# Optimization experiments

Measured on AMD Instinct MI355X. Metric: run time of the kernel, lower is better.

## Reference

```python
import jax, jax.numpy as jnp
import numpy as np

D_MODEL = 1024
NHEAD = 16
HEAD_DIM = D_MODEL // NHEAD
LN_EPS = 1e-5
ROPE_BASE = 10000.0


def _rope_cos_sin(n, head_dim):
    inv_freq = 1.0 / (ROPE_BASE ** (jnp.arange(0, head_dim, 2, dtype=jnp.float32) / head_dim))
    t = jnp.arange(n, dtype=jnp.float32)
    freqs = jnp.outer(t, inv_freq)  # (N, head_dim//2)
    return jnp.cos(freqs), jnp.sin(freqs)


def _apply_rope(x, cos, sin):
    # x: (B, H, N, hd); cos/sin: (N, hd//2)
    B, H, N, hd = x.shape
    xr = x.reshape(B, H, N, hd // 2, 2)
    x0, x1 = xr[..., 0], xr[..., 1]
    c = cos[None, None]
    s = sin[None, None]
    rot = jnp.stack([x0 * c - x1 * s, x0 * s + x1 * c], axis=-1)
    return rot.reshape(B, H, N, hd)


def setup_inputs() -> dict:
    key = jax.random.key(0)
    ks = jax.random.split(key, 6)
    D = D_MODEL
    scale = 1.0 / np.sqrt(D)
    x = jax.random.normal(ks[0], (2, 2048, D), dtype=jnp.float32)
    Wq = jax.random.normal(ks[1], (D, D), dtype=jnp.float32) * scale
    Wk = jax.random.normal(ks[2], (D, D), dtype=jnp.float32) * scale
    Wv = jax.random.normal(ks[3], (D, D), dtype=jnp.float32) * scale
    Wo = jax.random.normal(ks[4], (D, D), dtype=jnp.float32) * scale
    bq = jnp.zeros((D,), jnp.float32)
    bk = jnp.zeros((D,), jnp.float32)
    bv = jnp.zeros((D,), jnp.float32)
    bo = jnp.zeros((D,), jnp.float32)
    ln_w = jnp.ones((D,), jnp.float32)
    ln_b = jnp.zeros((D,), jnp.float32)
    return {"x": x, "ln_w": ln_w, "ln_b": ln_b, "Wq": Wq, "bq": bq,
            "Wk": Wk, "bk": bk, "Wv": Wv, "bv": bv, "Wo": Wo, "bo": bo}


def reference(x, ln_w, ln_b, Wq, bq, Wk, bk, Wv, bv, Wo, bo):
    B, N, D = x.shape
    H, hd = NHEAD, HEAD_DIM
    # LayerNorm
    mu = jnp.mean(x, axis=-1, keepdims=True)
    var = jnp.mean(jnp.square(x - mu), axis=-1, keepdims=True)
    xn = (x - mu) * jax.lax.rsqrt(var + LN_EPS) * ln_w + ln_b
    # QKV projections -> (B, H, N, hd)
    def proj(W, b):
        return (xn @ W.T + b).reshape(B, N, H, hd).transpose(0, 2, 1, 3)
    q = proj(Wq, bq)
    k = proj(Wk, bk)
    v = proj(Wv, bv)
    cos, sin = _rope_cos_sin(N, hd)
    q = _apply_rope(q, cos, sin)
    k = _apply_rope(k, cos, sin)
    scores = jnp.einsum('bhqd,bhkd->bhqk', q, k) / jnp.sqrt(jnp.float32(hd))
    attn = jax.nn.softmax(scores, axis=-1)
    out = jnp.einsum('bhqk,bhkd->bhqd', attn, v)
    out = out.transpose(0, 2, 1, 3).reshape(B, N, D)
    return x + out @ Wo.T + bo
```

## Files before the change

kernel.cpp:

```cpp
#include <hip/hip_runtime.h>


#define SEQ 2048
#define LN_EPS 1e-5f

using short8 = __attribute__((ext_vector_type(8))) short;
using f32x4  = __attribute__((ext_vector_type(4))) float;
using f32x16 = __attribute__((ext_vector_type(16))) float;

__device__ __forceinline__ unsigned short f2bf(float f) {
  union { float f; unsigned u; } v; v.f = f;
  unsigned r = v.u + 0x7FFFu + ((v.u >> 16) & 1u);
  return (unsigned short)(r >> 16);
}

__device__ __forceinline__ void async16(const void* g, void* l) {
  __builtin_amdgcn_global_load_lds(
      (const __attribute__((address_space(1))) void*)g,
      (__attribute__((address_space(3))) void*)l, 16, 0, 0);
}

__global__ __launch_bounds__(256) void prep_kernel(
    const float* __restrict__ x, const float* __restrict__ lnw, const float* __restrict__ lnb,
    const float* __restrict__ wq, const float* __restrict__ wk,
    const float* __restrict__ wv, const float* __restrict__ wo,
    unsigned short* __restrict__ wqkv, unsigned short* __restrict__ wob,
    unsigned short* __restrict__ xn, float2* __restrict__ tab) {
  const int b = blockIdx.x, t = threadIdx.x;
  if (b < 4096) {
    const int gid = b * 256 + t;
    const int m = gid >> 18, e4 = gid & 262143;
    const float* src = (m == 0) ? wq : (m == 1) ? wk : (m == 2) ? wv : wo;
    const float4 v = ((const float4*)src)[e4];
    ushort4 o; o.x = f2bf(v.x); o.y = f2bf(v.y); o.z = f2bf(v.z); o.w = f2bf(v.w);
    if (m < 3) ((ushort4*)wqkv)[(size_t)m * 262144 + e4] = o;
    else       ((ushort4*)wob)[e4] = o;
  } else if (b < 8192) {
    const int row = b - 4096;
    const float4 v = ((const float4*)(x + (size_t)row * 1024))[t];
    float s  = v.x + v.y + v.z + v.w;
    float s2 = v.x * v.x + v.y * v.y + v.z * v.z + v.w * v.w;
#pragma unroll
    for (int off = 32; off >= 1; off >>= 1) {
      s  += __shfl_xor(s, off);
      s2 += __shfl_xor(s2, off);
    }
    __shared__ float red[8];
    const int lane = t & 63, wave = t >> 6;
    if (lane == 0) { red[wave] = s; red[4 + wave] = s2; }
    __syncthreads();
    s  = red[0] + red[1] + red[2] + red[3];
    s2 = red[4] + red[5] + red[6] + red[7];
    const float mu   = s * (1.0f / 1024.0f);
    const float var  = s2 * (1.0f / 1024.0f) - mu * mu;
    const float rstd = rsqrtf(var + LN_EPS);
    const float4 wv4 = ((const float4*)lnw)[t];
    const float4 bv4 = ((const float4*)lnb)[t];
    ushort4 o;
    o.x = f2bf((v.x - mu) * rstd * wv4.x + bv4.x);
    o.y = f2bf((v.y - mu) * rstd * wv4.y + bv4.y);
    o.z = f2bf((v.z - mu) * rstd * wv4.z + bv4.z);
    o.w = f2bf((v.w - mu) * rstd * wv4.w + bv4.w);
    ((ushort4*)xn)[(size_t)row * 256 + t] = o;
  } else {
    const int gid = (b - 8192) * 256 + t;
    const int pos = gid >> 5, ip = gid & 31;
    const float invf = exp2f((float)ip * -0.4152410118609203f);
    const float fr = (float)pos * invf;
    tab[gid] = make_float2(cosf(fr), sinf(fr));
  }
}

__global__ __launch_bounds__(256, 3) void gemm_qkv_kernel(
    const unsigned short* __restrict__ A,
    const unsigned short* __restrict__ Bw,
    const float* __restrict__ bq, const float* __restrict__ bk, const float* __restrict__ bv,
    const float2* __restrict__ tab,
    unsigned short* __restrict__ qb, unsigned short* __restrict__ kbg,
    unsigned short* __restrict__ vtb) {
  __shared__ unsigned short lA[128 * 64];
  __shared__ unsigned short lB[128 * 64];
  const int tid = threadIdx.x;
  const int lane = tid & 63, wave = tid >> 6;
  const int lr = lane & 15, quad = lane >> 4;
  const int wm = (wave >> 1) * 64, wn = (wave & 1) * 64;
  const int n0 = blockIdx.x * 128, m0 = blockIdx.y * 128;
  const int r7 = lr & 7;
  const int lrow = lane >> 3, lcg = (lane & 7) ^ lrow;
  const int lin = blockIdx.y * gridDim.x + blockIdx.x;
  const int phase = ((lin >> 8) * 5) & 15;

  f32x4 acc[4][4];
#pragma unroll
  for (int i = 0; i < 4; ++i)
#pragma unroll
    for (int j = 0; j < 4; ++j) acc[i][j] = (f32x4){0.f, 0.f, 0.f, 0.f};

  for (int kt = 0; kt < 16; ++kt) {
    const int kofs = ((kt + phase) & 15) * 64;
    __syncthreads();
#pragma unroll
    for (int c = 0; c < 4; ++c) {
      const int chunk = wave * 4 + c;
      const int grow = chunk * 8 + lrow;
      async16(&A[(size_t)(m0 + grow) * 1024 + kofs + lcg * 8], &lA[chunk * 512]);
      async16(&Bw[(size_t)(n0 + grow) * 1024 + kofs + lcg * 8], &lB[chunk * 512]);
    }
    __syncthreads();
#pragma unroll
    for (int kk = 0; kk < 2; ++kk) {
      short8 a[4], b[4];
#pragma unroll
      for (int i = 0; i < 4; ++i)
        a[i] = *(const short8*)&lA[(wm + i * 16 + lr) * 64 + ((kk * 4 + quad) ^ r7) * 8];
#pragma unroll
      for (int j = 0; j < 4; ++j)
        b[j] = *(const short8*)&lB[(wn + j * 16 + lr) * 64 + ((kk * 4 + quad) ^ r7) * 8];
#pragma unroll
      for (int i = 0; i < 4; ++i)
#pragma unroll
        for (int j = 0; j < 4; ++j)
          acc[i][j] = __builtin_amdgcn_mfma_f32_16x16x32_bf16(a[i], b[j], acc[i][j], 0, 0, 0);
    }
  }

  const int which = n0 >> 10;
  const float* bias = (which == 0) ? bq : (which == 1) ? bk : bv;
  const float qs = (which == 0) ? 0.18033688011112042f : 1.0f;
#pragma unroll
  for (int i = 0; i < 4; ++i)
#pragma unroll
    for (int j = 0; j < 4; ++j)
#pragma unroll
      for (int r = 0; r < 4; ++r) {
        const int row = m0 + wm + i * 16 + quad * 4 + r;
        const int col = n0 + wn + j * 16 + lr;
        const int c = col & 1023;
        float val = (acc[i][j][r] + bias[c]) * qs;
        const int head = c >> 6, hd_i = c & 63;
        const int b_ = row >> 11, pos = row & 2047;
        if (which < 2) {
          const float partner = __shfl_xor(val, 1);
          const float2 cs = tab[(pos << 5) + (hd_i >> 1)];
          val = val * cs.x + partner * ((lane & 1) ? cs.y : -cs.y);
        }
        if (which == 2) {
          vtb[((size_t)((b_ * 16 + head) * 64 + hd_i)) * SEQ + pos] = f2bf(val);
        } else {
          const size_t didx = ((size_t)((b_ * 16 + head) * SEQ + pos)) * 64 + hd_i;
          if (which == 0) qb[didx] = f2bf(val);
          else            kbg[didx] = f2bf(val);
        }
      }
}

__global__ __launch_bounds__(256, 3) void gemm_o_kernel(
    const unsigned short* __restrict__ A,
    const unsigned short* __restrict__ Bw,
    const float* __restrict__ bo, const float* __restrict__ xres, float* __restrict__ out) {
  __shared__ unsigned short lA[128 * 64];
  __shared__ unsigned short lB[64 * 64];
  const int tid = threadIdx.x;
  const int lane = tid & 63, wave = tid >> 6;
  const int lr = lane & 15, quad = lane >> 4;
  const int wm = (wave >> 1) * 64, wn = (wave & 1) * 32;
  const int n0 = blockIdx.x * 64, m0 = blockIdx.y * 128;
  const int r7 = lr & 7;
  const int lrow = lane >> 3, lcg = (lane & 7) ^ lrow;
  const int lin = blockIdx.y * gridDim.x + blockIdx.x;
  const int phase = ((lin >> 8) * 8) & 15;

  f32x4 acc[4][2];
#pragma unroll
  for (int i = 0; i < 4; ++i)
#pragma unroll
    for (int j = 0; j < 2; ++j) acc[i][j] = (f32x4){0.f, 0.f, 0.f, 0.f};

  for (int kt = 0; kt < 16; ++kt) {
    const int kofs = ((kt + phase) & 15) * 64;
    __syncthreads();
#pragma unroll
    for (int c = 0; c < 4; ++c) {
      const int chunk = wave * 4 + c;
      const int grow = chunk * 8 + lrow;
      async16(&A[(size_t)(m0 + grow) * 1024 + kofs + lcg * 8], &lA[chunk * 512]);
    }
#pragma unroll
    for (int c = 0; c < 2; ++c) {
      const int chunk = wave * 2 + c;
      const int grow = chunk * 8 + lrow;
      async16(&Bw[(size_t)(n0 + grow) * 1024 + kofs + lcg * 8], &lB[chunk * 512]);
    }
    __syncthreads();
#pragma unroll
    for (int kk = 0; kk < 2; ++kk) {
      short8 a[4], b[2];
#pragma unroll
      for (int i = 0; i < 4; ++i)
        a[i] = *(const short8*)&lA[(wm + i * 16 + lr) * 64 + ((kk * 4 + quad) ^ r7) * 8];
#pragma unroll
      for (int j = 0; j < 2; ++j)
        b[j] = *(const short8*)&lB[(wn + j * 16 + lr) * 64 + ((kk * 4 + quad) ^ r7) * 8];
#pragma unroll
      for (int i = 0; i < 4; ++i)
#pragma unroll
        for (int j = 0; j < 2; ++j)
          acc[i][j] = __builtin_amdgcn_mfma_f32_16x16x32_bf16(a[i], b[j], acc[i][j], 0, 0, 0);
    }
  }

#pragma unroll
  for (int i = 0; i < 4; ++i)
#pragma unroll
    for (int j = 0; j < 2; ++j)
#pragma unroll
      for (int r = 0; r < 4; ++r) {
        const int row = m0 + wm + i * 16 + quad * 4 + r;
        const int col = n0 + wn + j * 16 + lr;
        const size_t idx = (size_t)row * 1024 + col;
        out[idx] = acc[i][j][r] + bo[col] + xres[idx];
      }
}

__global__ __launch_bounds__(256) void attn_kernel(
    const unsigned short* __restrict__ qg, const unsigned short* __restrict__ kg,
    const unsigned short* __restrict__ vtg, unsigned short* __restrict__ ao) {
  __shared__ unsigned short lK[2][128 * 64];
  __shared__ unsigned short lV[2][64 * 128];
  const int tid = threadIdx.x;
  const int lane = tid & 63, w = tid >> 6;
  const int l31 = lane & 31, hb = lane >> 5, l7 = lane & 7;
  const int bh = blockIdx.x >> 4, qt = blockIdx.x & 15;
  const int q0w = qt * 128 + w * 32;
  const int phase = ((blockIdx.x >> 8) * 8) & 15;
  const unsigned short* Q  = qg + (size_t)bh * SEQ * 64;
  const unsigned short* K  = kg + (size_t)bh * SEQ * 64;
  const unsigned short* VT = vtg + (size_t)bh * 64 * SEQ;

  short8 qf[4];
#pragma unroll
  for (int c = 0; c < 4; ++c)
    qf[c] = *(const short8*)&Q[(size_t)(q0w + l31) * 64 + c * 16 + hb * 8];

  f32x16 o[2];
#pragma unroll
  for (int dh = 0; dh < 2; ++dh)
#pragma unroll
    for (int r = 0; r < 16; ++r) o[dh][r] = 0.f;
  float ls = 0.f;

  const int k_row = lane >> 3, k_g = (lane & 7) ^ (k_row & 7);
  const int v_row = lane >> 4, v_g0 = lane & 15;

  {
    const int kb0 = (phase & 15) * 128;
#pragma unroll
    for (int c = 0; c < 4; ++c) {
      const int kc = w * 4 + c;
      const int krow = kc * 8 + k_row;
      async16(&K[(size_t)(kb0 + krow) * 64 + k_g * 8], &lK[0][kc * 512]);
      const int vrow = kc * 4 + v_row;
      const int vg = v_g0 ^ (vrow & 7);
      async16(&VT[(size_t)vrow * SEQ + kb0 + vg * 8], &lV[0][kc * 512]);
    }
  }
  __syncthreads();

  for (int kt = 0; kt < 16; ++kt) {
    const int cur = kt & 1;
    if (kt < 15) {
      const int kb0 = ((kt + 1 + phase) & 15) * 128;
#pragma unroll
      for (int c = 0; c < 4; ++c) {
        const int kc = w * 4 + c;
        const int krow = kc * 8 + k_row;
        async16(&K[(size_t)(kb0 + krow) * 64 + k_g * 8], &lK[cur ^ 1][kc * 512]);
        const int vrow = kc * 4 + v_row;
        const int vg = v_g0 ^ (vrow & 7);
        async16(&VT[(size_t)vrow * SEQ + kb0 + vg * 8], &lV[cur ^ 1][kc * 512]);
      }
    }
    const unsigned short* Kb = lK[cur];
    const unsigned short* Vb = lV[cur];

#pragma unroll
    for (int kb2 = 0; kb2 < 4; ++kb2) {
      f32x16 sv;
#pragma unroll
      for (int r = 0; r < 16; ++r) sv[r] = 0.f;
      const int key = kb2 * 32 + l31;
#pragma unroll
      for (int c = 0; c < 4; ++c) {
        const short8 af = *(const short8*)&Kb[key * 64 + (((c * 2 + hb) ^ l7) << 3)];
        sv = __builtin_amdgcn_mfma_f32_32x32x16_bf16(af, qf[c], sv, 0, 0, 0);
      }
      unsigned wp[8];
#pragma unroll
      for (int p = 0; p < 8; ++p) {
        union { float f; unsigned u; } e0, e1;
        e0.f = __builtin_amdgcn_exp2f(sv[2 * p]);
        e1.f = __builtin_amdgcn_exp2f(sv[2 * p + 1]);
        ls += e0.f + e1.f;
        wp[p] = __builtin_amdgcn_perm(e1.u, e0.u, 0x07060302u);
      }
      unsigned wlo[8], whi[8];
#pragma unroll
      for (int p = 0; p < 8; ++p) {
        auto rr = __builtin_amdgcn_permlane32_swap(wp[p], wp[p], false, false);
        wlo[p] = rr[0]; whi[p] = rr[1];
      }
#pragma unroll
      for (int cl = 0; cl < 2; ++cl) {
        const int pb = cl * 4;
        union { unsigned u[4]; short8 s; } pf;
        pf.u[0] = hb ? wlo[pb + 2] : wlo[pb + 0];
        pf.u[1] = hb ? wlo[pb + 3] : wlo[pb + 1];
        pf.u[2] = hb ? whi[pb + 2] : whi[pb + 0];
        pf.u[3] = hb ? whi[pb + 3] : whi[pb + 1];
        const int chunk = kb2 * 2 + cl;
#pragma unroll
        for (int dh = 0; dh < 2; ++dh) {
          const int d = dh * 32 + l31;
          const short8 vf = *(const short8*)&Vb[d * 128 + (((chunk * 2 + hb) ^ l7) << 3)];
          o[dh] = __builtin_amdgcn_mfma_f32_32x32x16_bf16(pf.s, vf, o[dh], 0, 0, 0);
        }
      }
    }
    __syncthreads();
  }

  union { float f; unsigned u; } lsu; lsu.f = ls;
  auto lr2 = __builtin_amdgcn_permlane32_swap(lsu.u, lsu.u, false, false);
  union { unsigned u; float f; } la, lb2; la.u = lr2[0]; lb2.u = lr2[1];
  const float rl = 1.0f / (la.f + lb2.f);

  const int b_ = bh >> 4, h = bh & 15;
#pragma unroll
  for (int r = 0; r < 16; ++r) {
    const int m = (r & 3) + 8 * (r >> 2) + 4 * hb;
    const float rlv = __shfl(rl, m);
    const int row = q0w + m;
#pragma unroll
    for (int dh = 0; dh < 2; ++dh)
      ao[(size_t)(b_ * SEQ + row) * 1024 + h * 64 + dh * 32 + l31] = f2bf(o[dh][r] * rlv);
  }
}

extern "C" void kernel_launch(void* const* d_in, const int* in_sizes, int n_in,
                              void* d_out, int out_size, void* d_ws, size_t ws_size,
                              hipStream_t stream) {
  const float* x   = (const float*)d_in[0];
  const float* lnw = (const float*)d_in[1];
  const float* lnb = (const float*)d_in[2];
  const float* Wq  = (const float*)d_in[3];
  const float* bq  = (const float*)d_in[4];
  const float* Wk  = (const float*)d_in[5];
  const float* bk  = (const float*)d_in[6];
  const float* Wv  = (const float*)d_in[7];
  const float* bv  = (const float*)d_in[8];
  const float* Wo  = (const float*)d_in[9];
  const float* bo  = (const float*)d_in[10];
  float* out = (float*)d_out;

  char* ws = (char*)d_ws;
  unsigned short* wqkv = (unsigned short*)(ws);
  unsigned short* wob  = (unsigned short*)(ws + 6291456);
  unsigned short* xn   = (unsigned short*)(ws + 8388608);
  unsigned short* qb   = (unsigned short*)(ws + 16777216);
  unsigned short* kbuf = (unsigned short*)(ws + 25165824);
  unsigned short* vtb  = (unsigned short*)(ws + 33554432);
  unsigned short* ao   = (unsigned short*)(ws + 41943040);
  float2*         tab  = (float2*)(ws + 50331648);

  hipLaunchKernelGGL(prep_kernel, dim3(8448), dim3(256), 0, stream,
                     x, lnw, lnb, Wq, Wk, Wv, Wo, wqkv, wob, xn, tab);
  hipLaunchKernelGGL(gemm_qkv_kernel, dim3(24, 32), dim3(256), 0, stream,
                     xn, wqkv, bq, bk, bv, tab, qb, kbuf, vtb);
  hipLaunchKernelGGL(attn_kernel, dim3(512), dim3(256), 0, stream, qb, kbuf, vtb, ao);
  hipLaunchKernelGGL(gemm_o_kernel, dim3(16, 32), dim3(256), 0, stream,
                     ao, wob, bo, x, out);
}
```

Baseline: 223.9 us.

## Split attention keys across two wave groups with register-staged LDS loads

The attention kernel now launches 512 threads per block. Two groups of four waves each process half of the key sequence for the same 128 queries, and their partial outputs and row sums are combined through LDS at the end. K/V tiles are now loaded into registers and written to LDS in a pre-permuted fragment layout after compute, replacing the async global-to-LDS loads with XOR swizzle. The goal is more waves per CU and better latency hiding, at the cost of a final reduction, an extra barrier, and more register pressure from the staged loads.

```diff
diff --git a/kernel.cpp b/kernel.cpp
--- a/kernel.cpp
+++ b/kernel.cpp
@@ -222,16 +222,17 @@
       }
 }
 
-__global__ __launch_bounds__(256) void attn_kernel(
+__global__ __launch_bounds__(512, 4) void attn_kernel(
     const unsigned short* __restrict__ qg, const unsigned short* __restrict__ kg,
     const unsigned short* __restrict__ vtg, unsigned short* __restrict__ ao) {
-  __shared__ unsigned short lK[2][128 * 64];
-  __shared__ unsigned short lV[2][64 * 128];
+  __shared__ unsigned short lKf[2][2][4096];
+  __shared__ unsigned short lVf[2][2][4096];
   const int tid = threadIdx.x;
   const int lane = tid & 63, w = tid >> 6;
-  const int l31 = lane & 31, hb = lane >> 5, l7 = lane & 7;
+  const int ws = w & 3, kh = w >> 2;
+  const int l31 = lane & 31, hb = lane >> 5;
   const int bh = blockIdx.x >> 4, qt = blockIdx.x & 15;
-  const int q0w = qt * 128 + w * 32;
+  const int q0w = qt * 128 + ws * 32;
   const int phase = ((blockIdx.x >> 8) * 8) & 15;
   const unsigned short* Q  = qg + (size_t)bh * SEQ * 64;
   const unsigned short* K  = kg + (size_t)bh * SEQ * 64;
@@ -249,49 +250,50 @@
     for (int r = 0; r < 16; ++r) o[dh][r] = 0.f;
   float ls = 0.f;
 
-  const int k_row = lane >> 3, k_g = (lane & 7) ^ (k_row & 7);
-  const int v_row = lane >> 4, v_g0 = lane & 15;
-
+  const int srow = ws * 16 + (lane & 15);
+  const int g0 = (lane >> 4) * 2;
+  const int khbase = kh * 1024;
+  const unsigned short* Ksrc = K + (size_t)(khbase + srow) * 64 + g0 * 8;
+  const unsigned short* Vsrc = VT + (size_t)srow * SEQ + khbase + g0 * 8;
+  const int kds0 = (((srow >> 5) * 8 + g0) * 32 + (srow & 31)) * 8;
+  const int kds1 = kds0 + 256;
+  const int vds0 = ((g0 * 2 + (srow >> 5)) * 32 + (srow & 31)) * 8;
+  const int vds1 = vds0 + 512;
+
+  short8 R0, R1, R2, R3;
   {
-    const int kb0 = (phase & 15) * 128;
-#pragma unroll
-    for (int c = 0; c < 4; ++c) {
-      const int kc = w * 4 + c;
-      const int krow = kc * 8 + k_row;
-      async16(&K[(size_t)(kb0 + krow) * 64 + k_g * 8], &lK[0][kc * 512]);
-      const int vrow = kc * 4 + v_row;
-      const int vg = v_g0 ^ (vrow & 7);
-      async16(&VT[(size_t)vrow * SEQ + kb0 + vg * 8], &lV[0][kc * 512]);
-    }
+    const int kb = phase;
+    R0 = *(const short8*)(Ksrc + kb * 4096);
+    R1 = *(const short8*)(Ksrc + kb * 4096 + 8);
+    R2 = *(const short8*)(Vsrc + kb * 64);
+    R3 = *(const short8*)(Vsrc + kb * 64 + 8);
+    *(short8*)&lKf[0][kh][kds0] = R0;
+    *(short8*)&lKf[0][kh][kds1] = R1;
+    *(short8*)&lVf[0][kh][vds0] = R2;
+    *(short8*)&lVf[0][kh][vds1] = R3;
   }
   __syncthreads();
 
   for (int kt = 0; kt < 16; ++kt) {
     const int cur = kt & 1;
     if (kt < 15) {
-      const int kb0 = ((kt + 1 + phase) & 15) * 128;
+      const int kb = (kt + 1 + phase) & 15;
+      R0 = *(const short8*)(Ksrc + kb * 4096);
+      R1 = *(const short8*)(Ksrc + kb * 4096 + 8);
+      R2 = *(const short8*)(Vsrc + kb * 64);
+      R3 = *(const short8*)(Vsrc + kb * 64 + 8);
+    }
+    const unsigned short* Kb = &lKf[cur][kh][0];
+    const unsigned short* Vb = &lVf[cur][kh][0];
+
+#pragma unroll
+    for (int kb2 = 0; kb2 < 2; ++kb2) {
+      f32x16 sv;
+#pragma unroll
+      for (int r = 0; r < 16; ++r) sv[r] = 0.f;
 #pragma unroll
       for (int c = 0; c < 4; ++c) {
-        const int kc = w * 4 + c;
-        const int krow = kc * 8 + k_row;
-        async16(&K[(size_t)(kb0 + krow) * 64 + k_g * 8], &lK[cur ^ 1][kc * 512]);
-        const int vrow = kc * 4 + v_row;
-        const int vg = v_g0 ^ (vrow & 7);
-        async16(&VT[(size_t)vrow * SEQ + kb0 + vg * 8], &lV[cur ^ 1][kc * 512]);
-      }
-    }
-    const unsigned short* Kb = lK[cur];
-    const unsigned short* Vb = lV[cur];
-
-#pragma unroll
-    for (int kb2 = 0; kb2 < 4; ++kb2) {
-      f32x16 sv;
-#pragma unroll
-      for (int r = 0; r < 16; ++r) sv[r] = 0.f;
-      const int key = kb2 * 32 + l31;
-#pragma unroll
-      for (int c = 0; c < 4; ++c) {
-        const short8 af = *(const short8*)&Kb[key * 64 + (((c * 2 + hb) ^ l7) << 3)];
+        const short8 af = *(const short8*)&Kb[((kb2 * 8 + c * 2 + hb) * 32 + l31) * 8];
         sv = __builtin_amdgcn_mfma_f32_32x32x16_bf16(af, qf[c], sv, 0, 0, 0);
       }
       unsigned wp[8];
@@ -317,14 +319,20 @@
         pf.u[1] = hb ? wlo[pb + 3] : wlo[pb + 1];
         pf.u[2] = hb ? whi[pb + 2] : whi[pb + 0];
         pf.u[3] = hb ? whi[pb + 3] : whi[pb + 1];
-        const int chunk = kb2 * 2 + cl;
+        const int ch = kb2 * 2 + cl;
 #pragma unroll
         for (int dh = 0; dh < 2; ++dh) {
-          const int d = dh * 32 + l31;
-          const short8 vf = *(const short8*)&Vb[d * 128 + (((chunk * 2 + hb) ^ l7) << 3)];
+          const short8 vf = *(const short8*)&Vb[(((ch * 2 + hb) * 2 + dh) * 32 + l31) * 8];
           o[dh] = __builtin_amdgcn_mfma_f32_32x32x16_bf16(pf.s, vf, o[dh], 0, 0, 0);
         }
       }
+    }
+
+    if (kt < 15) {
+      *(short8*)&lKf[cur ^ 1][kh][kds0] = R0;
+      *(short8*)&lKf[cur ^ 1][kh][kds1] = R1;
+      *(short8*)&lVf[cur ^ 1][kh][vds0] = R2;
+      *(short8*)&lVf[cur ^ 1][kh][vds1] = R3;
     }
     __syncthreads();
   }
@@ -332,17 +340,33 @@
   union { float f; unsigned u; } lsu; lsu.f = ls;
   auto lr2 = __builtin_amdgcn_permlane32_swap(lsu.u, lsu.u, false, false);
   union { unsigned u; float f; } la, lb2; la.u = lr2[0]; lb2.u = lr2[1];
-  const float rl = 1.0f / (la.f + lb2.f);
-
-  const int b_ = bh >> 4, h = bh & 15;
-#pragma unroll
-  for (int r = 0; r < 16; ++r) {
-    const int m = (r & 3) + 8 * (r >> 2) + 4 * hb;
-    const float rlv = __shfl(rl, m);
-    const int row = q0w + m;
+  const float lsH = la.f + lb2.f;
+
+  float* osh = (float*)&lKf[0][0][0];
+  float* lsh = (float*)&lVf[0][0][0];
+  if (kh == 1) {
 #pragma unroll
     for (int dh = 0; dh < 2; ++dh)
-      ao[(size_t)(b_ * SEQ + row) * 1024 + h * 64 + dh * 32 + l31] = f2bf(o[dh][r] * rlv);
+#pragma unroll
+      for (int r = 0; r < 16; ++r)
+        osh[((ws * 2 + dh) * 16 + r) * 64 + lane] = o[dh][r];
+    lsh[ws * 64 + lane] = lsH;
+  }
+  __syncthreads();
+  if (kh == 0) {
+    const float rl = 1.0f / (lsH + lsh[ws * 64 + lane]);
+    const int b_ = bh >> 4, h = bh & 15;
+#pragma unroll
+    for (int r = 0; r < 16; ++r) {
+      const int m = (r & 3) + 8 * (r >> 2) + 4 * hb;
+      const float rlv = __shfl(rl, m);
+      const int row = q0w + m;
+#pragma unroll
+      for (int dh = 0; dh < 2; ++dh) {
+        const float ov = o[dh][r] + osh[((ws * 2 + dh) * 16 + r) * 64 + lane];
+        ao[(size_t)(b_ * SEQ + row) * 1024 + h * 64 + dh * 32 + l31] = f2bf(ov * rlv);
+      }
+    }
   }
 }
 
@@ -376,7 +400,7 @@
                      x, lnw, lnb, Wq, Wk, Wv, Wo, wqkv, wob, xn, tab);
   hipLaunchKernelGGL(gemm_qkv_kernel, dim3(24, 32), dim3(256), 0, stream,
                      xn, wqkv, bq, bk, bv, tab, qb, kbuf, vtb);
-  hipLaunchKernelGGL(attn_kernel, dim3(512), dim3(256), 0, stream, qb, kbuf, vtb, ao);
+  hipLaunchKernelGGL(attn_kernel, dim3(512), dim3(512), 0, stream, qb, kbuf, vtb, ao);
   hipLaunchKernelGGL(gemm_o_kernel, dim3(16, 32), dim3(256), 0, stream,
                      ao, wob, bo, x, out);
 }
```

New measurement: 214.6 us. -4.1%, faster.
